# Optimization experiments

Hardware: AMD Instinct MI355X
Metric: run time of the kernel (lower is better)

Reference implementation:

```python
import jax, jax.numpy as jnp
import numpy as np

H = 1024   # hidden_dim
D = 256    # dynamics_dim
L = 2      # gru layers
BS = 1024  # batch
T = 256    # max_len
# activation layout over D: softmax[0:32], softmax[32:47], sigmoid[47:48], sigmoid[48:256]
CAT1 = 32
CAT2_SM_END = 47

def setup_inputs():
    key = jax.random.key(0)
    ks = jax.random.split(key, 12)
    s = 0.02
    return {
        "embed": jax.random.normal(ks[0], (BS, H * (1 + L)), jnp.float32),
        "dynamics": jax.random.uniform(ks[1], (BS, T, D), jnp.float32),
        "seq_len": T,
        "W_ih0": s * jax.random.normal(ks[2], (3 * H, H + D), jnp.float32),
        "W_hh0": s * jax.random.normal(ks[3], (3 * H, H), jnp.float32),
        "b_ih0": s * jax.random.normal(ks[4], (3 * H,), jnp.float32),
        "b_hh0": s * jax.random.normal(ks[5], (3 * H,), jnp.float32),
        "W_ih1": s * jax.random.normal(ks[6], (3 * H, H), jnp.float32),
        "W_hh1": s * jax.random.normal(ks[7], (3 * H, H), jnp.float32),
        "b_ih1": s * jax.random.normal(ks[8], (3 * H,), jnp.float32),
        "b_hh1": s * jax.random.normal(ks[9], (3 * H,), jnp.float32),
        "W_fc": s * jax.random.normal(ks[10], (D, H), jnp.float32),
        "b_fc": s * jax.random.normal(ks[11], (D,), jnp.float32),
    }

def gru_cell(inp, h, W_ih, W_hh, b_ih, b_hh):
    # PyTorch GRU cell math
    gi = inp @ W_ih.T + b_ih          # (bs, 3H)
    gh = h @ W_hh.T + b_hh            # (bs, 3H)
    r = jax.nn.sigmoid(gi[:, :H] + gh[:, :H])
    z = jax.nn.sigmoid(gi[:, H:2 * H] + gh[:, H:2 * H])
    n = jnp.tanh(gi[:, 2 * H:] + r * gh[:, 2 * H:])
    return (1.0 - z) * n + z * h

def apply_activation(x):
    # mirrors processors layout: cat(32), cat-missing(15 softmax + 1 sigmoid), cont(208 sigmoid)
    return jnp.concatenate([
        jax.nn.softmax(x[:, :CAT1], axis=-1),
        jax.nn.softmax(x[:, CAT1:CAT2_SM_END], axis=-1),
        jax.nn.sigmoid(x[:, CAT2_SM_END:]),
    ], axis=-1)

def reference(embed, dynamics, seq_len, W_ih0, W_hh0, b_ih0, b_hh0,
              W_ih1, W_hh1, b_ih1, b_hh1, W_fc, b_fc):
    glob = embed[:, :H]                      # (bs, H)
    h0 = embed[:, H:2 * H]                   # layer-0 initial hidden
    h1 = embed[:, 2 * H:3 * H]               # layer-1 initial hidden
    x0 = dynamics[:, 0, :]                   # (bs, D)

    def step(carry, _):
        x, h0, h1 = carry
        inp = jnp.concatenate([glob, jax.lax.stop_gradient(x)], axis=-1)  # x.detach()
        h0n = gru_cell(inp, h0, W_ih0, W_hh0, b_ih0, b_hh0)
        h1n = gru_cell(h0n, h1, W_ih1, W_hh1, b_ih1, b_hh1)
        out = apply_activation(h1n @ W_fc.T + b_fc)  # (bs, D)
        return (out, h0n, h1n), out

    _, res = jax.lax.scan(step, (x0, h0, h1), None, length=T)
    res = jnp.transpose(res, (1, 0, 2))  # (bs, max_len, D)
    return res
```

## Files before the change

### kernel.cpp

```cpp
#include <hip/hip_runtime.h>

#define HH    1024
#define DD    256
#define BSB   1024
#define TT    256
#define N3H   3072
#define CAT1  32
#define CAT2E 47

typedef unsigned short u16;
typedef short bf16x8 __attribute__((ext_vector_type(8)));
typedef float f32x4  __attribute__((ext_vector_type(4)));

__device__ __forceinline__ u16 f2bf(float f) {
  unsigned int x = __float_as_uint(f);
  unsigned int lsb = (x >> 16) & 1u;
  x += 0x7fffu + lsb;
  return (u16)(x >> 16);
}

__device__ __forceinline__ void gload_lds16(const u16* src, u16* lds) {
  __builtin_amdgcn_global_load_lds(
      (const __attribute__((address_space(1))) void*)src,
      (__attribute__((address_space(3))) void*)lds, 16, 0, 0);
}

struct GArg {
  const u16* A; int lda; int K;
  const u16* B; int ldb; int N;
  float* C; int ldc;
  const float* bias;
  const float* addend;
};

#define BM 128
#define BN 128
#define BK 64

__global__ __launch_bounds__(256, 3) void gemm_bt3(GArg ga, GArg gb)
{
  GArg g = (blockIdx.z == 0) ? ga : gb;
  const int colBase = blockIdx.x * BN;
  if (colBase >= g.N) return;
  const int rowBase = blockIdx.y * BM;

  __shared__ __align__(16) u16 As[BM * BK];
  __shared__ __align__(16) u16 Bs[BN * BK];

  const int tid  = threadIdx.x;
  const int wave = tid >> 6;
  const int lane = tid & 63;
  const int q    = lane >> 4;
  const int l16  = lane & 15;
  const int waveRow = (wave >> 1) * 64;
  const int waveCol = (wave & 1) * 64;

  const int  srow = wave * 8 + (lane >> 3);
  const int  sswz = ((lane & 7) ^ (lane >> 3)) << 3;
  const u16* aptr = g.A + (size_t)(rowBase + srow) * g.lda + sswz;
  const u16* bptr = g.B + (size_t)(colBase + srow) * g.ldb + sswz;
  const size_t astep = (size_t)32 * g.lda;
  const size_t bstep = (size_t)32 * g.ldb;
  u16* aldst = &As[wave << 9];
  u16* bldst = &Bs[wave << 9];

  f32x4 acc[4][4];
  #pragma unroll
  for (int i = 0; i < 4; ++i)
    #pragma unroll
    for (int j = 0; j < 4; ++j)
      acc[i][j] = (f32x4){0.f, 0.f, 0.f, 0.f};

  for (int k0 = 0; k0 < g.K; k0 += BK) {
    __syncthreads();
    #pragma unroll
    for (int i = 0; i < 4; ++i) {
      gload_lds16(aptr + k0 + (size_t)i * astep, aldst + (i << 11));
      gload_lds16(bptr + k0 + (size_t)i * bstep, bldst + (i << 11));
    }
    __syncthreads();

    #pragma unroll
    for (int ks = 0; ks < 2; ++ks) {
      bf16x8 af[4], bfr[4];
      const int kb = (ks << 2) + q;
      #pragma unroll
      for (int mi = 0; mi < 4; ++mi) {
        int r = waveRow + mi * 16 + l16;
        af[mi] = *(const bf16x8*)&As[(r << 6) + ((kb ^ (l16 & 7)) << 3)];
      }
      #pragma unroll
      for (int ni = 0; ni < 4; ++ni) {
        int r = waveCol + ni * 16 + l16;
        bfr[ni] = *(const bf16x8*)&Bs[(r << 6) + ((kb ^ (l16 & 7)) << 3)];
      }
      #pragma unroll
      for (int mi = 0; mi < 4; ++mi)
        #pragma unroll
        for (int ni = 0; ni < 4; ++ni)
          acc[mi][ni] = __builtin_amdgcn_mfma_f32_16x16x32_bf16(af[mi], bfr[ni], acc[mi][ni], 0, 0, 0);
    }
  }

  #pragma unroll
  for (int mi = 0; mi < 4; ++mi) {
    #pragma unroll
    for (int ni = 0; ni < 4; ++ni) {
      #pragma unroll
      for (int r = 0; r < 4; ++r) {
        int row = rowBase + waveRow + mi * 16 + q * 4 + r;
        int col = colBase + waveCol + ni * 16 + l16;
        float v = acc[mi][ni][r];
        if (g.bias)   v += g.bias[col];
        if (g.addend) v += g.addend[(size_t)row * g.ldc + col];
        g.C[(size_t)row * g.ldc + col] = v;
      }
    }
  }
}

__device__ __forceinline__ float gate1f(float gir, float ghr, float giz, float ghz,
                                        float gin, float ghn, float hv) {
  float r = 1.f / (1.f + expf(-(gir + ghr)));
  float z = 1.f / (1.f + expf(-(giz + ghz)));
  float n = tanhf(gin + r * ghn);
  return (1.f - z) * n + z * hv;
}

__global__ void gate_kernel(const float4* __restrict__ GI, const float4* __restrict__ GH,
                            float4* __restrict__ h, ushort4* __restrict__ hbf)
{
  int idx = blockIdx.x * blockDim.x + threadIdx.x;
  int b = idx >> 8, m = idx & 255;
  size_t base = (size_t)b * 768;
  float4 gir = GI[base + m], giz = GI[base + 256 + m], gin = GI[base + 512 + m];
  float4 ghr = GH[base + m], ghz = GH[base + 256 + m], ghn = GH[base + 512 + m];
  float4 hv = h[idx];
  float4 hn;
  hn.x = gate1f(gir.x, ghr.x, giz.x, ghz.x, gin.x, ghn.x, hv.x);
  hn.y = gate1f(gir.y, ghr.y, giz.y, ghz.y, gin.y, ghn.y, hv.y);
  hn.z = gate1f(gir.z, ghr.z, giz.z, ghz.z, gin.z, ghn.z, hv.z);
  hn.w = gate1f(gir.w, ghr.w, giz.w, ghz.w, gin.w, ghn.w, hv.w);
  h[idx] = hn;
  ushort4 hb;
  hb.x = f2bf(hn.x); hb.y = f2bf(hn.y); hb.z = f2bf(hn.z); hb.w = f2bf(hn.w);
  hbf[idx] = hb;
}

__global__ void act_kernel(const float* __restrict__ logits,
                           float* __restrict__ out, u16* __restrict__ xbf, int t)
{
  int b = blockIdx.x;
  int d = threadIdx.x;
  __shared__ float sv[DD];
  float v = logits[(size_t)b * DD + d];
  sv[d] = v;
  __syncthreads();
  float res;
  if (d < CAT1) {
    float m = -1e30f;
    for (int j = 0; j < CAT1; ++j) m = fmaxf(m, sv[j]);
    float s = 0.f;
    for (int j = 0; j < CAT1; ++j) s += expf(sv[j] - m);
    res = expf(v - m) / s;
  } else if (d < CAT2E) {
    float m = -1e30f;
    for (int j = CAT1; j < CAT2E; ++j) m = fmaxf(m, sv[j]);
    float s = 0.f;
    for (int j = CAT1; j < CAT2E; ++j) s += expf(sv[j] - m);
    res = expf(v - m) / s;
  } else {
    res = 1.f / (1.f + expf(-v));
  }
  out[((size_t)b * TT + t) * DD + d] = res;
  xbf[b * DD + d] = f2bf(res);
}

__global__ void convert_kernel(const float* __restrict__ src, u16* __restrict__ dst, int n)
{
  int i = blockIdx.x * blockDim.x + threadIdx.x;
  if (i < n) dst[i] = f2bf(src[i]);
}

__global__ void prep_state(const float* __restrict__ embed, const float* __restrict__ dyn,
                           u16* __restrict__ globbf,
                           float* __restrict__ h0, u16* __restrict__ h0bf,
                           float* __restrict__ h1, u16* __restrict__ h1bf,
                           u16* __restrict__ xbf)
{
  int idx = blockIdx.x * blockDim.x + threadIdx.x;
  int b = idx >> 10, j = idx & 1023;
  const float* e = embed + (size_t)b * 3072;
  globbf[idx] = f2bf(e[j]);
  float v0 = e[1024 + j]; h0[idx] = v0; h0bf[idx] = f2bf(v0);
  float v1 = e[2048 + j]; h1[idx] = v1; h1bf[idx] = f2bf(v1);
  if (j < DD) {
    xbf[b * DD + j] = f2bf(dyn[(size_t)b * (TT * DD) + j]);
  }
}

extern "C" void kernel_launch(void* const* d_in, const int* in_sizes, int n_in,
                              void* d_out, int out_size, void* d_ws, size_t ws_size,
                              hipStream_t stream)
{
  const float* embed = (const float*)d_in[0];
  const float* dyn   = (const float*)d_in[1];
  const float* W_ih0 = (const float*)d_in[3];
  const float* W_hh0 = (const float*)d_in[4];
  const float* b_ih0 = (const float*)d_in[5];
  const float* b_hh0 = (const float*)d_in[6];
  const float* W_ih1 = (const float*)d_in[7];
  const float* W_hh1 = (const float*)d_in[8];
  const float* b_ih1 = (const float*)d_in[9];
  const float* b_hh1 = (const float*)d_in[10];
  const float* W_fc  = (const float*)d_in[11];
  const float* b_fc  = (const float*)d_in[12];
  float* out = (float*)d_out;

  char* ws = (char*)d_ws;
  size_t off = 0;
  auto carve = [&](size_t bytes) -> void* {
    void* p = ws + off;
    off += (bytes + 255) & ~(size_t)255;
    return p;
  };
  u16* Wih0b = (u16*)carve((size_t)N3H * 1280 * 2);
  u16* Whh0b = (u16*)carve((size_t)N3H * HH * 2);
  u16* Wih1b = (u16*)carve((size_t)N3H * HH * 2);
  u16* Whh1b = (u16*)carve((size_t)N3H * HH * 2);
  u16* Wfcb  = (u16*)carve((size_t)DD * HH * 2);
  u16* globb = (u16*)carve((size_t)BSB * HH * 2);
  u16* xbf   = (u16*)carve((size_t)BSB * DD * 2);
  float* h0f = (float*)carve((size_t)BSB * HH * 4);
  float* h1f = (float*)carve((size_t)BSB * HH * 4);
  u16* h0b   = (u16*)carve((size_t)BSB * HH * 2);
  u16* h1b   = (u16*)carve((size_t)BSB * HH * 2);
  float* Gglob  = (float*)carve((size_t)BSB * N3H * 4);
  float* GI     = (float*)carve((size_t)BSB * N3H * 4);
  float* GH0f   = (float*)carve((size_t)BSB * N3H * 4);
  float* GH1f   = (float*)carve((size_t)BSB * N3H * 4);
  float* logits = (float*)carve((size_t)BSB * DD * 4);
  (void)ws_size;

  {
    int n;
    n = N3H * 1280; convert_kernel<<<(n + 255) / 256, 256, 0, stream>>>(W_ih0, Wih0b, n);
    n = N3H * HH;   convert_kernel<<<(n + 255) / 256, 256, 0, stream>>>(W_hh0, Whh0b, n);
    n = N3H * HH;   convert_kernel<<<(n + 255) / 256, 256, 0, stream>>>(W_ih1, Wih1b, n);
    n = N3H * HH;   convert_kernel<<<(n + 255) / 256, 256, 0, stream>>>(W_hh1, Whh1b, n);
    n = DD * HH;    convert_kernel<<<(n + 255) / 256, 256, 0, stream>>>(W_fc, Wfcb, n);
  }
  prep_state<<<(BSB * HH) / 256, 256, 0, stream>>>(embed, dyn, globb, h0f, h0b, h1f, h1b, xbf);

  const dim3 G1(N3H / BN, BSB / BM, 1);
  const dim3 G2(N3H / BN, BSB / BM, 2);

  {
    GArg g{globb, HH, HH, Wih0b, 1280, N3H, Gglob, N3H, b_ih0, nullptr};
    gemm_bt3<<<G1, 256, 0, stream>>>(g, g);
  }
  {
    GArg ga{h0b, HH, HH, Whh0b, HH, N3H, GH0f, N3H, b_hh0, nullptr};
    GArg gb{h1b, HH, HH, Whh1b, HH, N3H, GH1f, N3H, b_hh1, nullptr};
    gemm_bt3<<<G2, 256, 0, stream>>>(ga, gb);
  }
  {
    GArg g{xbf, DD, DD, Wih0b + HH, 1280, N3H, GI, N3H, nullptr, Gglob};
    gemm_bt3<<<G1, 256, 0, stream>>>(g, g);
  }

  for (int t = 0; t < TT; ++t) {
    bool last = (t == TT - 1);

    gate_kernel<<<(BSB * HH / 4) / 256, 256, 0, stream>>>(
        (const float4*)GI, (const float4*)GH0f, (float4*)h0f, (ushort4*)h0b);

    {
      GArg gi{h0b, HH, HH, Wih1b, HH, N3H, GI, N3H, b_ih1, nullptr};
      GArg gh{h0b, HH, HH, Whh0b, HH, N3H, GH0f, N3H, b_hh0, nullptr};
      gemm_bt3<<<last ? G1 : G2, 256, 0, stream>>>(gi, gh);
    }

    gate_kernel<<<(BSB * HH / 4) / 256, 256, 0, stream>>>(
        (const float4*)GI, (const float4*)GH1f, (float4*)h1f, (ushort4*)h1b);

    {
      GArg gc{h1b, HH, HH, Wfcb, HH, DD, logits, DD, b_fc, nullptr};
      GArg gh{h1b, HH, HH, Whh1b, HH, N3H, GH1f, N3H, b_hh1, nullptr};
      gemm_bt3<<<last ? G1 : G2, 256, 0, stream>>>(gc, gh);
    }

    act_kernel<<<BSB, DD, 0, stream>>>(logits, out, xbf, t);

    if (!last) {
      GArg g{xbf, DD, DD, Wih0b + HH, 1280, N3H, GI, N3H, nullptr, Gglob};
      gemm_bt3<<<G1, 256, 0, stream>>>(g, g);
    }
  }
}
```

Measured before the change: 25.18 ms.

## Double-buffer GEMM LDS loads and fuse output activation into FC GEMM

The GEMM now keeps two LDS stages and issues async global-to-LDS loads two K-tiles ahead, waiting with vmcnt counters, so memory latency overlaps the MFMA work instead of a load, sync, compute loop. Launch bounds drop to 2 blocks per CU to make room for the doubled shared memory. The softmax/sigmoid activation is fused into the FC GEMM epilogue using wave shuffles, which removes the separate act kernel launch and the logits round trip each timestep. The costs are lower occupancy and more complex epilogue code.

After: 25.10 ms. Within noise of the previous version (-0.3%).

```diff
diff --git a/kernel.cpp b/kernel.cpp
--- a/kernel.cpp
+++ b/kernel.cpp
@@ -31,21 +31,25 @@
   float* C; int ldc;
   const float* bias;
   const float* addend;
+  float* out;
+  u16* xout;
+  int tstep;
+  int act;
 };
 
 #define BM 128
 #define BN 128
 #define BK 64
 
-__global__ __launch_bounds__(256, 3) void gemm_bt3(GArg ga, GArg gb)
+__global__ __launch_bounds__(256, 2) void gemm_bt4(GArg ga, GArg gb)
 {
   GArg g = (blockIdx.z == 0) ? ga : gb;
   const int colBase = blockIdx.x * BN;
   if (colBase >= g.N) return;
   const int rowBase = blockIdx.y * BM;
 
-  __shared__ __align__(16) u16 As[BM * BK];
-  __shared__ __align__(16) u16 Bs[BN * BK];
+  __shared__ __align__(16) u16 As[2][BM * BK];
+  __shared__ __align__(16) u16 Bs[2][BN * BK];
 
   const int tid  = threadIdx.x;
   const int wave = tid >> 6;
@@ -61,8 +65,7 @@
   const u16* bptr = g.B + (size_t)(colBase + srow) * g.ldb + sswz;
   const size_t astep = (size_t)32 * g.lda;
   const size_t bstep = (size_t)32 * g.ldb;
-  u16* aldst = &As[wave << 9];
-  u16* bldst = &Bs[wave << 9];
+  const int ldoff = wave << 9;
 
   f32x4 acc[4][4];
   #pragma unroll
@@ -71,14 +74,28 @@
     for (int j = 0; j < 4; ++j)
       acc[i][j] = (f32x4){0.f, 0.f, 0.f, 0.f};
 
-  for (int k0 = 0; k0 < g.K; k0 += BK) {
-    __syncthreads();
-    #pragma unroll
-    for (int i = 0; i < 4; ++i) {
-      gload_lds16(aptr + k0 + (size_t)i * astep, aldst + (i << 11));
-      gload_lds16(bptr + k0 + (size_t)i * bstep, bldst + (i << 11));
-    }
-    __syncthreads();
+  const int nk = g.K >> 6;
+
+  #pragma unroll
+  for (int i = 0; i < 4; ++i) {
+    gload_lds16(aptr + (size_t)i * astep, &As[0][ldoff + (i << 11)]);
+    gload_lds16(bptr + (size_t)i * bstep, &Bs[0][ldoff + (i << 11)]);
+  }
+  #pragma unroll
+  for (int i = 0; i < 4; ++i) {
+    gload_lds16(aptr + 64 + (size_t)i * astep, &As[1][ldoff + (i << 11)]);
+    gload_lds16(bptr + 64 + (size_t)i * bstep, &Bs[1][ldoff + (i << 11)]);
+  }
+
+  for (int k = 0; k < nk; ++k) {
+    const int cur = k & 1;
+    if (k < nk - 1) {
+      asm volatile("s_waitcnt vmcnt(8)" ::: "memory");
+    } else {
+      asm volatile("s_waitcnt vmcnt(0)" ::: "memory");
+    }
+    __builtin_amdgcn_s_barrier();
+    __builtin_amdgcn_sched_barrier(0);
 
     #pragma unroll
     for (int ks = 0; ks < 2; ++ks) {
@@ -87,12 +104,12 @@
       #pragma unroll
       for (int mi = 0; mi < 4; ++mi) {
         int r = waveRow + mi * 16 + l16;
-        af[mi] = *(const bf16x8*)&As[(r << 6) + ((kb ^ (l16 & 7)) << 3)];
+        af[mi] = *(const bf16x8*)&As[cur][(r << 6) + ((kb ^ (l16 & 7)) << 3)];
       }
       #pragma unroll
       for (int ni = 0; ni < 4; ++ni) {
         int r = waveCol + ni * 16 + l16;
-        bfr[ni] = *(const bf16x8*)&Bs[(r << 6) + ((kb ^ (l16 & 7)) << 3)];
+        bfr[ni] = *(const bf16x8*)&Bs[cur][(r << 6) + ((kb ^ (l16 & 7)) << 3)];
       }
       #pragma unroll
       for (int mi = 0; mi < 4; ++mi)
@@ -100,6 +117,65 @@
         for (int ni = 0; ni < 4; ++ni)
           acc[mi][ni] = __builtin_amdgcn_mfma_f32_16x16x32_bf16(af[mi], bfr[ni], acc[mi][ni], 0, 0, 0);
     }
+
+    __builtin_amdgcn_sched_barrier(0);
+    __builtin_amdgcn_s_barrier();
+    __builtin_amdgcn_sched_barrier(0);
+    if (k + 2 < nk) {
+      const int k2 = (k + 2) << 6;
+      #pragma unroll
+      for (int i = 0; i < 4; ++i) {
+        gload_lds16(aptr + k2 + (size_t)i * astep, &As[cur][ldoff + (i << 11)]);
+        gload_lds16(bptr + k2 + (size_t)i * bstep, &Bs[cur][ldoff + (i << 11)]);
+      }
+    }
+  }
+
+  if (g.act) {
+    const bool smWave = (colBase + waveCol) == 0;
+    #pragma unroll
+    for (int mi = 0; mi < 4; ++mi) {
+      #pragma unroll
+      for (int r = 0; r < 4; ++r) {
+        const int row = rowBase + waveRow + mi * 16 + q * 4 + r;
+        float v[4];
+        #pragma unroll
+        for (int ni = 0; ni < 4; ++ni)
+          v[ni] = acc[mi][ni][r] + g.bias[colBase + waveCol + ni * 16 + l16];
+        float res[4];
+        if (smWave) {
+          float m1 = fmaxf(v[0], v[1]);
+          #pragma unroll
+          for (int msk = 1; msk < 16; msk <<= 1) m1 = fmaxf(m1, __shfl_xor(m1, msk));
+          float e0 = expf(v[0] - m1), e1 = expf(v[1] - m1);
+          float s1 = e0 + e1;
+          #pragma unroll
+          for (int msk = 1; msk < 16; msk <<= 1) s1 += __shfl_xor(s1, msk);
+          res[0] = e0 / s1;
+          res[1] = e1 / s1;
+          float mv = (l16 < 15) ? v[2] : -1e30f;
+          #pragma unroll
+          for (int msk = 1; msk < 16; msk <<= 1) mv = fmaxf(mv, __shfl_xor(mv, msk));
+          float e2 = expf(v[2] - mv);
+          float sv = (l16 < 15) ? e2 : 0.f;
+          #pragma unroll
+          for (int msk = 1; msk < 16; msk <<= 1) sv += __shfl_xor(sv, msk);
+          res[2] = (l16 < 15) ? (e2 / sv) : (1.f / (1.f + expf(-v[2])));
+          res[3] = 1.f / (1.f + expf(-v[3]));
+        } else {
+          #pragma unroll
+          for (int ni = 0; ni < 4; ++ni)
+            res[ni] = 1.f / (1.f + expf(-v[ni]));
+        }
+        #pragma unroll
+        for (int ni = 0; ni < 4; ++ni) {
+          const int col = colBase + waveCol + ni * 16 + l16;
+          g.out[((size_t)row * TT + g.tstep) * DD + col] = res[ni];
+          g.xout[row * DD + col] = f2bf(res[ni]);
+        }
+      }
+    }
+    return;
   }
 
   #pragma unroll
@@ -145,35 +221,6 @@
   ushort4 hb;
   hb.x = f2bf(hn.x); hb.y = f2bf(hn.y); hb.z = f2bf(hn.z); hb.w = f2bf(hn.w);
   hbf[idx] = hb;
-}
-
-__global__ void act_kernel(const float* __restrict__ logits,
-                           float* __restrict__ out, u16* __restrict__ xbf, int t)
-{
-  int b = blockIdx.x;
-  int d = threadIdx.x;
-  __shared__ float sv[DD];
-  float v = logits[(size_t)b * DD + d];
-  sv[d] = v;
-  __syncthreads();
-  float res;
-  if (d < CAT1) {
-    float m = -1e30f;
-    for (int j = 0; j < CAT1; ++j) m = fmaxf(m, sv[j]);
-    float s = 0.f;
-    for (int j = 0; j < CAT1; ++j) s += expf(sv[j] - m);
-    res = expf(v - m) / s;
-  } else if (d < CAT2E) {
-    float m = -1e30f;
-    for (int j = CAT1; j < CAT2E; ++j) m = fmaxf(m, sv[j]);
-    float s = 0.f;
-    for (int j = CAT1; j < CAT2E; ++j) s += expf(sv[j] - m);
-    res = expf(v - m) / s;
-  } else {
-    res = 1.f / (1.f + expf(-v));
-  }
-  out[((size_t)b * TT + t) * DD + d] = res;
-  xbf[b * DD + d] = f2bf(res);
 }
 
 __global__ void convert_kernel(const float* __restrict__ src, u16* __restrict__ dst, int n)
@@ -239,7 +286,6 @@
   float* GI     = (float*)carve((size_t)BSB * N3H * 4);
   float* GH0f   = (float*)carve((size_t)BSB * N3H * 4);
   float* GH1f   = (float*)carve((size_t)BSB * N3H * 4);
-  float* logits = (float*)carve((size_t)BSB * DD * 4);
   (void)ws_size;
 
   {
@@ -256,17 +302,17 @@
   const dim3 G2(N3H / BN, BSB / BM, 2);
 
   {
-    GArg g{globb, HH, HH, Wih0b, 1280, N3H, Gglob, N3H, b_ih0, nullptr};
-    gemm_bt3<<<G1, 256, 0, stream>>>(g, g);
+    GArg g{globb, HH, HH, Wih0b, 1280, N3H, Gglob, N3H, b_ih0, nullptr, nullptr, nullptr, 0, 0};
+    gemm_bt4<<<G1, 256, 0, stream>>>(g, g);
   }
   {
-    GArg ga{h0b, HH, HH, Whh0b, HH, N3H, GH0f, N3H, b_hh0, nullptr};
-    GArg gb{h1b, HH, HH, Whh1b, HH, N3H, GH1f, N3H, b_hh1, nullptr};
-    gemm_bt3<<<G2, 256, 0, stream>>>(ga, gb);
+    GArg ga{h0b, HH, HH, Whh0b, HH, N3H, GH0f, N3H, b_hh0, nullptr, nullptr, nullptr, 0, 0};
+    GArg gb{h1b, HH, HH, Whh1b, HH, N3H, GH1f, N3H, b_hh1, nullptr, nullptr, nullptr, 0, 0};
+    gemm_bt4<<<G2, 256, 0, stream>>>(ga, gb);
   }
   {
-    GArg g{xbf, DD, DD, Wih0b + HH, 1280, N3H, GI, N3H, nullptr, Gglob};
-    gemm_bt3<<<G1, 256, 0, stream>>>(g, g);
+    GArg g{xbf, DD, DD, Wih0b + HH, 1280, N3H, GI, N3H, nullptr, Gglob, nullptr, nullptr, 0, 0};
+    gemm_bt4<<<G1, 256, 0, stream>>>(g, g);
   }
 
   for (int t = 0; t < TT; ++t) {
@@ -276,25 +322,23 @@
         (const float4*)GI, (const float4*)GH0f, (float4*)h0f, (ushort4*)h0b);
 
     {
-      GArg gi{h0b, HH, HH, Wih1b, HH, N3H, GI, N3H, b_ih1, nullptr};
-      GArg gh{h0b, HH, HH, Whh0b, HH, N3H, GH0f, N3H, b_hh0, nullptr};
-      gemm_bt3<<<last ? G1 : G2, 256, 0, stream>>>(gi, gh);
+      GArg gi{h0b, HH, HH, Wih1b, HH, N3H, GI, N3H, b_ih1, nullptr, nullptr, nullptr, 0, 0};
+      GArg gh{h0b, HH, HH, Whh0b, HH, N3H, GH0f, N3H, b_hh0, nullptr, nullptr, nullptr, 0, 0};
+      gemm_bt4<<<last ? G1 : G2, 256, 0, stream>>>(gi, gh);
     }
 
     gate_kernel<<<(BSB * HH / 4) / 256, 256, 0, stream>>>(
         (const float4*)GI, (const float4*)GH1f, (float4*)h1f, (ushort4*)h1b);
 
     {
-      GArg gc{h1b, HH, HH, Wfcb, HH, DD, logits, DD, b_fc, nullptr};
-      GArg gh{h1b, HH, HH, Whh1b, HH, N3H, GH1f, N3H, b_hh1, nullptr};
-      gemm_bt3<<<last ? G1 : G2, 256, 0, stream>>>(gc, gh);
-    }
-
-    act_kernel<<<BSB, DD, 0, stream>>>(logits, out, xbf, t);
+      GArg gc{h1b, HH, HH, Wfcb, HH, DD, nullptr, DD, b_fc, nullptr, out, xbf, t, 1};
+      GArg gh{h1b, HH, HH, Whh1b, HH, N3H, GH1f, N3H, b_hh1, nullptr, nullptr, nullptr, 0, 0};
+      gemm_bt4<<<last ? G1 : G2, 256, 0, stream>>>(gc, gh);
+    }
 
     if (!last) {
-      GArg g{xbf, DD, DD, Wih0b + HH, 1280, N3H, GI, N3H, nullptr, Gglob};
-      gemm_bt3<<<G1, 256, 0, stream>>>(g, g);
-    }
-  }
-}
+      GArg g{xbf, DD, DD, Wih0b + HH, 1280, N3H, GI, N3H, nullptr, Gglob, nullptr, nullptr, 0, 0};
+      gemm_bt4<<<G1, 256, 0, stream>>>(g, g);
+    }
+  }
+}
```
